# Optimization experiments

Hardware: AMD Instinct MI355X
Metric: run time of the kernel (lower is better)

Reference implementation:

```python
import jax, jax.numpy as jnp
import numpy as np

N = 100000
E = 600000
NODE_DIM = 128
EDGE_DIM = 32
HIDDEN = 128  # must equal NODE_DIM (index_add_ into zeros_like(node_features))


def _linear_params(key, fan_in, fan_out):
    kw, kb = jax.random.split(key)
    bound = 1.0 / np.sqrt(fan_in)
    W = jax.random.uniform(kw, (fan_in, fan_out), minval=-bound, maxval=bound, dtype=jnp.float32)
    b = jax.random.uniform(kb, (fan_out,), minval=-bound, maxval=bound, dtype=jnp.float32)
    return W, b


def setup_inputs() -> dict:
    key = jax.random.key(0)
    ks = jax.random.split(key, 8)
    node_features = jax.random.normal(ks[0], (N, NODE_DIM), dtype=jnp.float32)
    edge_index = jax.random.randint(ks[1], (2, E), 0, N, dtype=jnp.int32)
    edge_features = jax.random.normal(ks[2], (E, EDGE_DIM), dtype=jnp.float32)
    m_W1, m_b1 = _linear_params(ks[3], 2 * NODE_DIM + EDGE_DIM, HIDDEN)
    m_W2, m_b2 = _linear_params(ks[4], HIDDEN, HIDDEN)
    a_W, a_b = _linear_params(ks[5], HIDDEN, 1)
    u_W1, u_b1 = _linear_params(ks[6], NODE_DIM + HIDDEN, HIDDEN)
    u_W2, u_b2 = _linear_params(ks[7], HIDDEN, NODE_DIM)
    return {
        "node_features": node_features,
        "edge_features": edge_features,
        "m_W1": m_W1, "m_b1": m_b1, "m_W2": m_W2, "m_b2": m_b2,
        "a_W": a_W, "a_b": a_b,
        "u_W1": u_W1, "u_b1": u_b1, "u_W2": u_W2, "u_b2": u_b2,
        "edge_index": edge_index,
    }


def reference(node_features, edge_features, m_W1, m_b1, m_W2, m_b2,
              a_W, a_b, u_W1, u_b1, u_W2, u_b2, edge_index):
    row, col = edge_index[0], edge_index[1]
    # gather endpoints + edge feats -> [E, 2*node_dim + edge_dim]
    msg_in = jnp.concatenate([node_features[row], node_features[col], edge_features], axis=-1)
    # message MLP
    h = jax.nn.relu(msg_in @ m_W1 + m_b1)
    messages = h @ m_W2 + m_b2  # [E, hidden]
    # global softmax over all edges (dim=0), per attention column (width 1)
    attn = jax.nn.softmax(messages @ a_W + a_b, axis=0)  # [E, 1]
    messages = messages * attn
    # scatter-add into destination nodes
    aggregated = jax.ops.segment_sum(messages, col, num_segments=node_features.shape[0])
    # update MLP + residual
    upd_in = jnp.concatenate([node_features, aggregated], axis=-1)
    u = jax.nn.relu(upd_in @ u_W1 + u_b1)
    updated = u @ u_W2 + u_b2
    return updated + node_features
```

## Files before the change

kernel.cpp:

```cpp
#include <hip/hip_runtime.h>
#include <hip/hip_bf16.h>
#include <hip/hip_fp8.h>
#include <stdint.h>

#define NN 100000
#define NE 600000
#define ND 128
#define ED 32
#define HID 128
#define SCANB 391
#define NB (NE / 192)

using short8 = __attribute__((ext_vector_type(8))) short;
using f32x4  = __attribute__((ext_vector_type(4))) float;
using f32x2  = __attribute__((ext_vector_type(2))) float;

__device__ __forceinline__ uint32_t f2bf(float f) {
  uint32_t u = __float_as_uint(f);
  return (u + 0x7FFFu + ((u >> 16) & 1u)) >> 16;
}
__device__ __forceinline__ short8 pack8(float4 a, float4 b) {
  short8 s;
  s[0] = (short)f2bf(a.x); s[1] = (short)f2bf(a.y);
  s[2] = (short)f2bf(a.z); s[3] = (short)f2bf(a.w);
  s[4] = (short)f2bf(b.x); s[5] = (short)f2bf(b.y);
  s[6] = (short)f2bf(b.z); s[7] = (short)f2bf(b.w);
  return s;
}

__device__ __forceinline__ uint8_t fp8_enc(float v) {
#if __has_builtin(__builtin_amdgcn_cvt_pk_fp8_f32)
  return (uint8_t)(__builtin_amdgcn_cvt_pk_fp8_f32(v, v, 0, false) & 0xFF);
#else
  __hip_fp8_e4m3 q(v);
  return q.__x;
#endif
}
__device__ __forceinline__ float2 fp8_dec2(uint32_t v) {
#if __has_builtin(__builtin_amdgcn_cvt_pk_f32_fp8)
  f32x2 r = __builtin_amdgcn_cvt_pk_f32_fp8((int)v, false);
  return make_float2(r[0], r[1]);
#else
  __hip_fp8_e4m3 qa, qb;
  qa.__x = (uint8_t)(v & 0xFF); qb.__x = (uint8_t)((v >> 8) & 0xFF);
  return make_float2((float)qa, (float)qb);
#endif
}

__global__ __launch_bounds__(256) void k_prep(
    const float* __restrict__ W1, const float* __restrict__ W2,
    const float* __restrict__ uW1, const float* __restrict__ uW2,
    short* __restrict__ W1p, short* __restrict__ W2p,
    short* __restrict__ U1p, short* __restrict__ U2p) {
  int o = blockIdx.x * 256 + threadIdx.x;
  const float* src; short* dst; int rel;
  if (o < 36864)      { rel = o;         src = W1;  dst = W1p; }
  else if (o < 53248) { rel = o - 36864; src = W2;  dst = W2p; }
  else if (o < 86016) { rel = o - 53248; src = uW1; dst = U1p; }
  else                { rel = o - 86016; src = uW2; dst = U2p; }
  int j = rel & 7, c16 = (rel >> 3) & 15, g = (rel >> 7) & 3, nt = (rel >> 9) & 7, c = rel >> 12;
  int k = c * 32 + g * 8 + j, n = nt * 16 + c16;
  dst[rel] = (short)f2bf(src[k * 128 + n]);
}

__global__ __launch_bounds__(256) void k_prep_nf(const float* __restrict__ nf,
                                                 short* __restrict__ nfb) {
  const int total = NN * ND / 8;
  for (int u = blockIdx.x * 256 + threadIdx.x; u < total; u += gridDim.x * 256) {
    const float* s = nf + (size_t)u * 8;
    float4 v0 = *(const float4*)s, v1 = *(const float4*)(s + 4);
    *(short8*)(nfb + (size_t)u * 8) = pack8(v0, v1);
  }
}

__global__ __launch_bounds__(256, 2) void k_edge_mfma(
    const short* __restrict__ nfb, const float* __restrict__ ef,
    const short* __restrict__ W1p, const float* __restrict__ b1,
    const short* __restrict__ W2p, const float* __restrict__ b2,
    const float* __restrict__ aW, const int* __restrict__ ei,
    const int* __restrict__ perm,
    uint8_t* __restrict__ msg8, float* __restrict__ logits) {
  __shared__ __align__(16) short sA[192 * 40];
  __shared__ __align__(16) short sB[4096];
  __shared__ __align__(16) short sH[192 * 136];
  __shared__ int sIdx[384];
  __shared__ int sPerm[192];
  uint8_t* const sF = (uint8_t*)sH;

  const int tid = threadIdx.x;
  const int wv = tid >> 6, ln = tid & 63, cr = ln & 15, gp = ln >> 4;
  const int e0 = blockIdx.x * 192;
  const int wrow = wv * 48;

  if (tid < 192) {
    sIdx[tid] = ei[e0 + tid];
    sIdx[192 + tid] = ei[NE + e0 + tid];
    sPerm[tid] = perm[e0 + tid];
  }

  float bia[8], aWr[8], bia2[8];
#pragma unroll
  for (int nt = 0; nt < 8; ++nt) {
    bia[nt] = b1[nt * 16 + cr];
    bia2[nt] = b2[nt * 16 + cr];
    aWr[nt] = aW[nt * 16 + cr];
  }
  f32x4 acc[3][8];
#pragma unroll
  for (int mt = 0; mt < 3; ++mt)
#pragma unroll
    for (int nt = 0; nt < 8; ++nt)
      acc[mt][nt] = (f32x4){bia[nt], bia[nt], bia[nt], bia[nt]};
  __syncthreads();

  for (int c = 0; c < 9; ++c) {
#pragma unroll
    for (int it = 0; it < 3; ++it) {
      int row = it * 64 + (tid >> 2), k8 = (tid & 3) * 8;
      if (c < 8) {
        const short* src = nfb + (size_t)sIdx[(c < 4 ? 0 : 192) + row] * ND +
                           (c & 3) * 32 + k8;
        *(short8*)&sA[row * 40 + k8] = *(const short8*)src;
      } else {
        const float* src = ef + (size_t)(e0 + row) * ED + k8;
        float4 v0 = *(const float4*)src, v1 = *(const float4*)(src + 4);
        *(short8*)&sA[row * 40 + k8] = pack8(v0, v1);
      }
    }
    {
      const short8* wsrc = (const short8*)(W1p + c * 4096);
      short8 t0 = wsrc[tid], t1 = wsrc[tid + 256];
      ((short8*)sB)[tid] = t0; ((short8*)sB)[tid + 256] = t1;
    }
    __syncthreads();
    short8 af[3];
#pragma unroll
    for (int mt = 0; mt < 3; ++mt)
      af[mt] = *(const short8*)&sA[(wrow + mt * 16 + cr) * 40 + gp * 8];
#pragma unroll
    for (int nt = 0; nt < 8; ++nt) {
      short8 bfr = *(const short8*)&sB[(nt * 4 + gp) * 128 + cr * 8];
#pragma unroll
      for (int mt = 0; mt < 3; ++mt)
        acc[mt][nt] = __builtin_amdgcn_mfma_f32_16x16x32_bf16(af[mt], bfr, acc[mt][nt], 0, 0, 0);
    }
    __syncthreads();
  }

#pragma unroll
  for (int mt = 0; mt < 3; ++mt)
#pragma unroll
    for (int nt = 0; nt < 8; ++nt)
#pragma unroll
      for (int rr = 0; rr < 4; ++rr)
        sH[(wrow + mt * 16 + gp * 4 + rr) * 136 + nt * 16 + cr] =
            (short)f2bf(fmaxf(acc[mt][nt][rr], 0.f));
  __syncthreads();

  f32x4 acc2[3][8];
#pragma unroll
  for (int mt = 0; mt < 3; ++mt)
#pragma unroll
    for (int nt = 0; nt < 8; ++nt)
      acc2[mt][nt] = (f32x4){bia2[nt], bia2[nt], bia2[nt], bia2[nt]};
  for (int c2 = 0; c2 < 4; ++c2) {
    {
      const short8* wsrc = (const short8*)(W2p + c2 * 4096);
      short8 t0 = wsrc[tid], t1 = wsrc[tid + 256];
      ((short8*)sB)[tid] = t0; ((short8*)sB)[tid + 256] = t1;
    }
    __syncthreads();
    short8 af[3];
#pragma unroll
    for (int mt = 0; mt < 3; ++mt)
      af[mt] = *(const short8*)&sH[(wrow + mt * 16 + cr) * 136 + c2 * 32 + gp * 8];
#pragma unroll
    for (int nt = 0; nt < 8; ++nt) {
      short8 bfr = *(const short8*)&sB[(nt * 4 + gp) * 128 + cr * 8];
#pragma unroll
      for (int mt = 0; mt < 3; ++mt)
        acc2[mt][nt] = __builtin_amdgcn_mfma_f32_16x16x32_bf16(af[mt], bfr, acc2[mt][nt], 0, 0, 0);
    }
    __syncthreads();
  }

#pragma unroll
  for (int mt = 0; mt < 3; ++mt)
#pragma unroll
    for (int rr = 0; rr < 4; ++rr) {
      float p = 0.f;
#pragma unroll
      for (int nt = 0; nt < 8; ++nt) p += acc2[mt][nt][rr] * aWr[nt];
      p += __shfl_xor(p, 1, 64);
      p += __shfl_xor(p, 2, 64);
      p += __shfl_xor(p, 4, 64);
      p += __shfl_xor(p, 8, 64);
      if (cr == 0) logits[sPerm[wrow + mt * 16 + gp * 4 + rr]] = p;
    }

#pragma unroll
  for (int mt = 0; mt < 3; ++mt)
#pragma unroll
    for (int nt = 0; nt < 8; ++nt)
#pragma unroll
      for (int rr = 0; rr < 4; ++rr)
        sF[(wrow + mt * 16 + gp * 4 + rr) * 136 + nt * 16 + cr] =
            fp8_enc(acc2[mt][nt][rr]);
  __syncthreads();
#pragma unroll
  for (int it = 0; it < 12; ++it) {
    int row = it * 16 + (tid >> 4), o8 = (tid & 15) * 8;
    *(uint2*)(msg8 + (size_t)sPerm[row] * HID + o8) = *(const uint2*)&sF[row * 136 + o8];
  }
}

__global__ __launch_bounds__(256, 2) void k_node_mfma(
    const float* __restrict__ nf, const short* __restrict__ nfb,
    const float* __restrict__ agg,
    const short* __restrict__ U1p, const float* __restrict__ b1,
    const short* __restrict__ U2p, const float* __restrict__ b2,
    float* __restrict__ out) {
  __shared__ __align__(16) short sA[192 * 40];
  __shared__ __align__(16) short sB[4096];
  __shared__ __align__(16) short sH[192 * 136];

  const int tid = threadIdx.x;
  const int wv = tid >> 6, ln = tid & 63, cr = ln & 15, gp = ln >> 4;
  const int n0 = blockIdx.x * 192;
  const int wrow = wv * 48;

  float bia[8], bia2[8];
#pragma unroll
  for (int nt = 0; nt < 8; ++nt) {
    bia[nt] = b1[nt * 16 + cr];
    bia2[nt] = b2[nt * 16 + cr];
  }
  f32x4 acc[3][8];
#pragma unroll
  for (int mt = 0; mt < 3; ++mt)
#pragma unroll
    for (int nt = 0; nt < 8; ++nt)
      acc[mt][nt] = (f32x4){bia[nt], bia[nt], bia[nt], bia[nt]};

  for (int c = 0; c < 8; ++c) {
#pragma unroll
    for (int it = 0; it < 3; ++it) {
      int row = it * 64 + (tid >> 2), k8 = (tid & 3) * 8;
      int n = n0 + row; if (n >= NN) n = NN - 1;
      if (c < 4) {
        *(short8*)&sA[row * 40 + k8] =
            *(const short8*)(nfb + (size_t)n * ND + c * 32 + k8);
      } else {
        const float* src = agg + (size_t)n * ND + (c - 4) * 32 + k8;
        float4 v0 = *(const float4*)src, v1 = *(const float4*)(src + 4);
        *(short8*)&sA[row * 40 + k8] = pack8(v0, v1);
      }
    }
    {
      const short8* wsrc = (const short8*)(U1p + c * 4096);
      short8 t0 = wsrc[tid], t1 = wsrc[tid + 256];
      ((short8*)sB)[tid] = t0; ((short8*)sB)[tid + 256] = t1;
    }
    __syncthreads();
    short8 af[3];
#pragma unroll
    for (int mt = 0; mt < 3; ++mt)
      af[mt] = *(const short8*)&sA[(wrow + mt * 16 + cr) * 40 + gp * 8];
#pragma unroll
    for (int nt = 0; nt < 8; ++nt) {
      short8 bfr = *(const short8*)&sB[(nt * 4 + gp) * 128 + cr * 8];
#pragma unroll
      for (int mt = 0; mt < 3; ++mt)
        acc[mt][nt] = __builtin_amdgcn_mfma_f32_16x16x32_bf16(af[mt], bfr, acc[mt][nt], 0, 0, 0);
    }
    __syncthreads();
  }

#pragma unroll
  for (int mt = 0; mt < 3; ++mt)
#pragma unroll
    for (int nt = 0; nt < 8; ++nt)
#pragma unroll
      for (int rr = 0; rr < 4; ++rr)
        sH[(wrow + mt * 16 + gp * 4 + rr) * 136 + nt * 16 + cr] =
            (short)f2bf(fmaxf(acc[mt][nt][rr], 0.f));
  __syncthreads();

  f32x4 acc2[3][8];
#pragma unroll
  for (int mt = 0; mt < 3; ++mt)
#pragma unroll
    for (int nt = 0; nt < 8; ++nt)
      acc2[mt][nt] = (f32x4){bia2[nt], bia2[nt], bia2[nt], bia2[nt]};
  for (int c2 = 0; c2 < 4; ++c2) {
    {
      const short8* wsrc = (const short8*)(U2p + c2 * 4096);
      short8 t0 = wsrc[tid], t1 = wsrc[tid + 256];
      ((short8*)sB)[tid] = t0; ((short8*)sB)[tid + 256] = t1;
    }
    __syncthreads();
    short8 af[3];
#pragma unroll
    for (int mt = 0; mt < 3; ++mt)
      af[mt] = *(const short8*)&sH[(wrow + mt * 16 + cr) * 136 + c2 * 32 + gp * 8];
#pragma unroll
    for (int nt = 0; nt < 8; ++nt) {
      short8 bfr = *(const short8*)&sB[(nt * 4 + gp) * 128 + cr * 8];
#pragma unroll
      for (int mt = 0; mt < 3; ++mt)
        acc2[mt][nt] = __builtin_amdgcn_mfma_f32_16x16x32_bf16(af[mt], bfr, acc2[mt][nt], 0, 0, 0);
    }
    __syncthreads();
  }

#pragma unroll
  for (int mt = 0; mt < 3; ++mt)
#pragma unroll
    for (int rr = 0; rr < 4; ++rr) {
      int n = n0 + wrow + mt * 16 + gp * 4 + rr;
      if (n < NN) {
#pragma unroll
        for (int nt = 0; nt < 8; ++nt) {
          int col = nt * 16 + cr;
          out[(size_t)n * ND + col] = acc2[mt][nt][rr] + nf[(size_t)n * ND + col];
        }
      }
    }
}

__device__ __forceinline__ void ms_combine(float& m, float& s, float m2, float s2) {
  float M = fmaxf(m, m2);
  s = s * expf(m - M) + s2 * expf(m2 - M);
  m = M;
}
__device__ __forceinline__ void ms_block_reduce(float& m, float& s) {
#pragma unroll
  for (int o = 1; o < 64; o <<= 1) {
    float m2 = __shfl_xor(m, o, 64), s2 = __shfl_xor(s, o, 64);
    ms_combine(m, s, m2, s2);
  }
  __shared__ float sm[4], ss[4];
  if ((threadIdx.x & 63) == 0) { sm[threadIdx.x >> 6] = m; ss[threadIdx.x >> 6] = s; }
  __syncthreads();
  m = sm[0]; s = ss[0];
  ms_combine(m, s, sm[1], ss[1]);
  ms_combine(m, s, sm[2], ss[2]);
  ms_combine(m, s, sm[3], ss[3]);
}
__global__ __launch_bounds__(256) void k_red_p(const float* __restrict__ logits,
                                               float* __restrict__ pmax,
                                               float* __restrict__ psum) {
  float m = -3.402823466e38f, s = 0.f;
  for (int i = blockIdx.x * 256 + threadIdx.x; i < NE; i += 1024 * 256) {
    float l = logits[i];
    if (l <= m) s += expf(l - m);
    else { s = s * expf(m - l) + 1.f; m = l; }
  }
  ms_block_reduce(m, s);
  if (threadIdx.x == 0) { pmax[blockIdx.x] = m; psum[blockIdx.x] = s; }
}
__global__ __launch_bounds__(256) void k_red_f(const float* __restrict__ pmax,
                                               const float* __restrict__ psum,
                                               float* __restrict__ red) {
  float m = pmax[threadIdx.x], s = psum[threadIdx.x];
  ms_combine(m, s, pmax[threadIdx.x + 256], psum[threadIdx.x + 256]);
  ms_combine(m, s, pmax[threadIdx.x + 512], psum[threadIdx.x + 512]);
  ms_combine(m, s, pmax[threadIdx.x + 768], psum[threadIdx.x + 768]);
  ms_block_reduce(m, s);
  if (threadIdx.x == 0) { red[0] = m; red[1] = 1.0f / s; }
}

__global__ __launch_bounds__(256) void k_zero_cnt(int* __restrict__ cnt) {
  int i = blockIdx.x * 256 + threadIdx.x;
  if (i < NN) cnt[i] = 0;
}
__global__ __launch_bounds__(256) void k_hist(const int* __restrict__ ei,
                                              int* __restrict__ cnt) {
  int e = blockIdx.x * 256 + threadIdx.x;
  if (e < NE) atomicAdd(&cnt[ei[NE + e]], 1);
}
__global__ __launch_bounds__(256) void k_scan_bsum(const int* __restrict__ cnt,
                                                   int* __restrict__ bsum) {
  int i = blockIdx.x * 256 + threadIdx.x;
  int v = (i < NN) ? cnt[i] : 0;
#pragma unroll
  for (int s = 1; s < 64; s <<= 1) v += __shfl_xor(v, s, 64);
  __shared__ int sv[4];
  if ((threadIdx.x & 63) == 0) sv[threadIdx.x >> 6] = v;
  __syncthreads();
  if (threadIdx.x == 0) bsum[blockIdx.x] = sv[0] + sv[1] + sv[2] + sv[3];
}
__global__ __launch_bounds__(512) void k_scan_boff(const int* __restrict__ bsum,
                                                   int* __restrict__ boff,
                                                   int* __restrict__ rowptr) {
  __shared__ int s[512];
  int t = threadIdx.x;
  int v = (t < SCANB) ? bsum[t] : 0;
  s[t] = v;
  __syncthreads();
  for (int off = 1; off < 512; off <<= 1) {
    int u = (t >= off) ? s[t - off] : 0;
    __syncthreads();
    s[t] += u;
    __syncthreads();
  }
  if (t < SCANB) boff[t] = s[t] - v;
  if (t == 0) rowptr[NN] = NE;
}
__global__ __launch_bounds__(256) void k_scan_final(int* __restrict__ cnt,
                                                    const int* __restrict__ boff,
                                                    int* __restrict__ rowptr) {
  __shared__ int s[256];
  int b = blockIdx.x, t = threadIdx.x, i = b * 256 + t;
  int v = (i < NN) ? cnt[i] : 0;
  s[t] = v;
  __syncthreads();
  for (int off = 1; off < 256; off <<= 1) {
    int u = (t >= off) ? s[t - off] : 0;
    __syncthreads();
    s[t] += u;
    __syncthreads();
  }
  int excl = s[t] - v + boff[b];
  if (i < NN) { rowptr[i] = excl; cnt[i] = excl; }
}
__global__ __launch_bounds__(256) void k_fill(const int* __restrict__ ei,
                                              int* __restrict__ cursor,
                                              int* __restrict__ perm) {
  int e = blockIdx.x * 256 + threadIdx.x;
  if (e >= NE) return;
  int c = ei[NE + e];
  int pos = atomicAdd(&cursor[c], 1);
  perm[e] = pos;
}

__global__ __launch_bounds__(256) void k_agg(
    const uint8_t* __restrict__ msg8, const float* __restrict__ logits,
    const int* __restrict__ rowptr, const float* __restrict__ red,
    float* __restrict__ out) {
  int n = blockIdx.x * 4 + (threadIdx.x >> 6);
  int lane = threadIdx.x & 63;
  if (n >= NN) return;
  float gm = red[0], inv = red[1];
  int i0 = rowptr[n], i1 = rowptr[n + 1];
  float a0 = 0.f, a1 = 0.f;
  for (int i = i0; i < i1; ++i) {
    float wt = expf(logits[i] - gm) * inv;
    uint32_t pk = *(const uint16_t*)(msg8 + (size_t)i * HID + lane * 2);
    float2 d = fp8_dec2(pk);
    a0 += wt * d.x;
    a1 += wt * d.y;
  }
  *(float2*)(out + (size_t)n * ND + lane * 2) = make_float2(a0, a1);
}

extern "C" void kernel_launch(void* const* d_in, const int* in_sizes, int n_in,
                              void* d_out, int out_size, void* d_ws, size_t ws_size,
                              hipStream_t stream) {
  const float* nf  = (const float*)d_in[0];
  const float* ef  = (const float*)d_in[1];
  const float* mW1 = (const float*)d_in[2];
  const float* mb1 = (const float*)d_in[3];
  const float* mW2 = (const float*)d_in[4];
  const float* mb2 = (const float*)d_in[5];
  const float* aW  = (const float*)d_in[6];
  const float* uW1 = (const float*)d_in[8];
  const float* ub1 = (const float*)d_in[9];
  const float* uW2 = (const float*)d_in[10];
  const float* ub2 = (const float*)d_in[11];
  const int*   ei  = (const int*)d_in[12];
  float* out = (float*)d_out;

  char* ws = (char*)d_ws;
  uint8_t* msg8 = (uint8_t*)ws;
  float* logits = (float*)(ws + 76800000);
  float* pmax = (float*)(ws + 79200000);
  float* psum = pmax + 1024;
  float* red  = psum + 1024;
  short* W1p = (short*)(ws + 79208256);
  short* W2p = W1p + 36864;
  short* U1p = W2p + 16384;
  short* U2p = U1p + 32768;
  int* rowptr = (int*)(ws + 79413056);
  int* cnt    = rowptr + (NN + 1);
  int* perm   = cnt + NN;
  int* bsum   = perm + NE;
  int* boff   = bsum + 512;
  short* nfb  = (short*)(ws + 82620000);

  k_prep<<<400, 256, 0, stream>>>(mW1, mW2, uW1, uW2, W1p, W2p, U1p, U2p);
  k_prep_nf<<<2048, 256, 0, stream>>>(nf, nfb);
  k_zero_cnt<<<SCANB, 256, 0, stream>>>(cnt);
  k_hist<<<(NE + 255) / 256, 256, 0, stream>>>(ei, cnt);
  k_scan_bsum<<<SCANB, 256, 0, stream>>>(cnt, bsum);
  k_scan_boff<<<1, 512, 0, stream>>>(bsum, boff, rowptr);
  k_scan_final<<<SCANB, 256, 0, stream>>>(cnt, boff, rowptr);
  k_fill<<<(NE + 255) / 256, 256, 0, stream>>>(ei, cnt, perm);
  k_edge_mfma<<<NB, 256, 0, stream>>>(nfb, ef, W1p, mb1, W2p, mb2, aW, ei, perm,
                                      msg8, logits);
  k_red_p<<<1024, 256, 0, stream>>>(logits, pmax, psum);
  k_red_f<<<1, 256, 0, stream>>>(pmax, psum, red);
  k_agg<<<(NN + 3) / 4, 256, 0, stream>>>(msg8, logits, rowptr, red, out);
  k_node_mfma<<<(NN + 191) / 192, 256, 0, stream>>>(nf, nfb, out, U1p, ub1, U2p, ub2, out);
}
```

Before: 340.2 us.

## Switch edge message MLP to FP8 MFMA with prefetched gathers and double-buffered weights

The edge MLP now uses FP8 e4m3 inputs and weights with the 16x16x32 fp8 MFMA instead of bf16. An fp8 copy of the node features is written in the prep kernel, and the row and column gathers for all 192 edges are loaded into shared memory once up front. Weight chunks are double-buffered, which removes one barrier per K chunk. This halves gather bytes and LDS traffic, but adds an extra fp8 node-feature write and lowers the precision of the messages and hidden activations.

```diff
diff --git a/kernel.cpp b/kernel.cpp
--- a/kernel.cpp
+++ b/kernel.cpp
@@ -48,44 +48,59 @@
 }
 
 __global__ __launch_bounds__(256) void k_prep(
-    const float* __restrict__ W1, const float* __restrict__ W2,
     const float* __restrict__ uW1, const float* __restrict__ uW2,
-    short* __restrict__ W1p, short* __restrict__ W2p,
     short* __restrict__ U1p, short* __restrict__ U2p) {
   int o = blockIdx.x * 256 + threadIdx.x;
   const float* src; short* dst; int rel;
-  if (o < 36864)      { rel = o;         src = W1;  dst = W1p; }
-  else if (o < 53248) { rel = o - 36864; src = W2;  dst = W2p; }
-  else if (o < 86016) { rel = o - 53248; src = uW1; dst = U1p; }
-  else                { rel = o - 86016; src = uW2; dst = U2p; }
+  if (o < 32768)      { rel = o;         src = uW1; dst = U1p; }
+  else if (o < 49152) { rel = o - 32768; src = uW2; dst = U2p; }
+  else return;
   int j = rel & 7, c16 = (rel >> 3) & 15, g = (rel >> 7) & 3, nt = (rel >> 9) & 7, c = rel >> 12;
   int k = c * 32 + g * 8 + j, n = nt * 16 + c16;
   dst[rel] = (short)f2bf(src[k * 128 + n]);
 }
 
+__global__ __launch_bounds__(256) void k_prep8(
+    const float* __restrict__ W1, const float* __restrict__ W2,
+    uint8_t* __restrict__ W1p8, uint8_t* __restrict__ W2p8) {
+  int o = blockIdx.x * 256 + threadIdx.x;
+  const float* src; uint8_t* dst; int rel;
+  if (o < 36864)      { rel = o;         src = W1; dst = W1p8; }
+  else if (o < 53248) { rel = o - 36864; src = W2; dst = W2p8; }
+  else return;
+  int j = rel & 7, c16 = (rel >> 3) & 15, g = (rel >> 7) & 3, nt = (rel >> 9) & 7, c = rel >> 12;
+  int k = c * 32 + g * 8 + j, n = nt * 16 + c16;
+  dst[rel] = fp8_enc(src[k * 128 + n]);
+}
+
 __global__ __launch_bounds__(256) void k_prep_nf(const float* __restrict__ nf,
-                                                 short* __restrict__ nfb) {
+                                                 short* __restrict__ nfb,
+                                                 uint8_t* __restrict__ nfb8) {
   const int total = NN * ND / 8;
   for (int u = blockIdx.x * 256 + threadIdx.x; u < total; u += gridDim.x * 256) {
     const float* s = nf + (size_t)u * 8;
     float4 v0 = *(const float4*)s, v1 = *(const float4*)(s + 4);
     *(short8*)(nfb + (size_t)u * 8) = pack8(v0, v1);
+    uint8_t b[8];
+    b[0] = fp8_enc(v0.x); b[1] = fp8_enc(v0.y); b[2] = fp8_enc(v0.z); b[3] = fp8_enc(v0.w);
+    b[4] = fp8_enc(v1.x); b[5] = fp8_enc(v1.y); b[6] = fp8_enc(v1.z); b[7] = fp8_enc(v1.w);
+    *(uint2*)(nfb8 + (size_t)u * 8) = *(const uint2*)b;
   }
 }
 
 __global__ __launch_bounds__(256, 2) void k_edge_mfma(
-    const short* __restrict__ nfb, const float* __restrict__ ef,
-    const short* __restrict__ W1p, const float* __restrict__ b1,
-    const short* __restrict__ W2p, const float* __restrict__ b2,
+    const uint8_t* __restrict__ nfb8, const float* __restrict__ ef,
+    const uint8_t* __restrict__ W1p8, const float* __restrict__ b1,
+    const uint8_t* __restrict__ W2p8, const float* __restrict__ b2,
     const float* __restrict__ aW, const int* __restrict__ ei,
     const int* __restrict__ perm,
     uint8_t* __restrict__ msg8, float* __restrict__ logits) {
-  __shared__ __align__(16) short sA[192 * 40];
-  __shared__ __align__(16) short sB[4096];
-  __shared__ __align__(16) short sH[192 * 136];
+  __shared__ __align__(16) uint8_t sRow[192 * 136];
+  __shared__ __align__(16) uint8_t sCol[192 * 136];
+  __shared__ __align__(16) uint8_t sEf[192 * 40];
+  __shared__ __align__(16) uint8_t sB8[2][4096];
   __shared__ int sIdx[384];
   __shared__ int sPerm[192];
-  uint8_t* const sF = (uint8_t*)sH;
 
   const int tid = threadIdx.x;
   const int wv = tid >> 6, ln = tid & 63, cr = ln & 15, gp = ln >> 4;
@@ -97,6 +112,30 @@
     sIdx[192 + tid] = ei[NE + e0 + tid];
     sPerm[tid] = perm[e0 + tid];
   }
+  __syncthreads();
+
+#pragma unroll
+  for (int it = 0; it < 24; ++it) {
+    int t = it * 256 + tid;
+    int side = t >= 3072;
+    int r = (t - side * 3072) >> 4;
+    int o = (t & 15) * 8;
+    const uint8_t* src = nfb8 + (size_t)sIdx[side * 192 + r] * ND + o;
+    uint8_t* dst = (side ? sCol : sRow) + r * 136 + o;
+    *(uint2*)dst = *(const uint2*)src;
+  }
+#pragma unroll
+  for (int it = 0; it < 3; ++it) {
+    int u = it * 256 + tid;
+    int r = u >> 2, o = (u & 3) * 8;
+    const float* src = ef + (size_t)(e0 + r) * ED + o;
+    float4 v0 = *(const float4*)src, v1 = *(const float4*)(src + 4);
+    uint8_t b[8];
+    b[0] = fp8_enc(v0.x); b[1] = fp8_enc(v0.y); b[2] = fp8_enc(v0.z); b[3] = fp8_enc(v0.w);
+    b[4] = fp8_enc(v1.x); b[5] = fp8_enc(v1.y); b[6] = fp8_enc(v1.z); b[7] = fp8_enc(v1.w);
+    *(uint2*)&sEf[r * 40 + o] = *(const uint2*)b;
+  }
+  *(uint4*)&sB8[0][tid * 16] = *(const uint4*)(W1p8 + tid * 16);
 
   float bia[8], aWr[8], bia2[8];
 #pragma unroll
@@ -114,35 +153,22 @@
   __syncthreads();
 
   for (int c = 0; c < 9; ++c) {
-#pragma unroll
-    for (int it = 0; it < 3; ++it) {
-      int row = it * 64 + (tid >> 2), k8 = (tid & 3) * 8;
-      if (c < 8) {
-        const short* src = nfb + (size_t)sIdx[(c < 4 ? 0 : 192) + row] * ND +
-                           (c & 3) * 32 + k8;
-        *(short8*)&sA[row * 40 + k8] = *(const short8*)src;
-      } else {
-        const float* src = ef + (size_t)(e0 + row) * ED + k8;
-        float4 v0 = *(const float4*)src, v1 = *(const float4*)(src + 4);
-        *(short8*)&sA[row * 40 + k8] = pack8(v0, v1);
-      }
-    }
-    {
-      const short8* wsrc = (const short8*)(W1p + c * 4096);
-      short8 t0 = wsrc[tid], t1 = wsrc[tid + 256];
-      ((short8*)sB)[tid] = t0; ((short8*)sB)[tid + 256] = t1;
-    }
-    __syncthreads();
-    short8 af[3];
-#pragma unroll
-    for (int mt = 0; mt < 3; ++mt)
-      af[mt] = *(const short8*)&sA[(wrow + mt * 16 + cr) * 40 + gp * 8];
+    if (c < 8)
+      *(uint4*)&sB8[(c + 1) & 1][tid * 16] =
+          *(const uint4*)(W1p8 + (c + 1) * 4096 + tid * 16);
+    const uint8_t* aSrc = (c < 4) ? (sRow + c * 32)
+                        : (c < 8) ? (sCol + (c - 4) * 32) : sEf;
+    const int pitch = (c == 8) ? 40 : 136;
+    long af0 = *(const long*)(aSrc + (wrow + cr) * pitch + gp * 8);
+    long af1 = *(const long*)(aSrc + (wrow + 16 + cr) * pitch + gp * 8);
+    long af2 = *(const long*)(aSrc + (wrow + 32 + cr) * pitch + gp * 8);
+    const uint8_t* bbuf = sB8[c & 1];
 #pragma unroll
     for (int nt = 0; nt < 8; ++nt) {
-      short8 bfr = *(const short8*)&sB[(nt * 4 + gp) * 128 + cr * 8];
-#pragma unroll
-      for (int mt = 0; mt < 3; ++mt)
-        acc[mt][nt] = __builtin_amdgcn_mfma_f32_16x16x32_bf16(af[mt], bfr, acc[mt][nt], 0, 0, 0);
+      long bfr = *(const long*)&bbuf[(nt * 4 + gp) * 128 + cr * 8];
+      acc[0][nt] = __builtin_amdgcn_mfma_f32_16x16x32_fp8_fp8(af0, bfr, acc[0][nt], 0, 0, 0);
+      acc[1][nt] = __builtin_amdgcn_mfma_f32_16x16x32_fp8_fp8(af1, bfr, acc[1][nt], 0, 0, 0);
+      acc[2][nt] = __builtin_amdgcn_mfma_f32_16x16x32_fp8_fp8(af2, bfr, acc[2][nt], 0, 0, 0);
     }
     __syncthreads();
   }
@@ -153,8 +179,9 @@
     for (int nt = 0; nt < 8; ++nt)
 #pragma unroll
       for (int rr = 0; rr < 4; ++rr)
-        sH[(wrow + mt * 16 + gp * 4 + rr) * 136 + nt * 16 + cr] =
-            (short)f2bf(fmaxf(acc[mt][nt][rr], 0.f));
+        sRow[(wrow + mt * 16 + gp * 4 + rr) * 136 + nt * 16 + cr] =
+            fp8_enc(fmaxf(acc[mt][nt][rr], 0.f));
+  *(uint4*)&sB8[0][tid * 16] = *(const uint4*)(W2p8 + tid * 16);
   __syncthreads();
 
   f32x4 acc2[3][8];
@@ -164,22 +191,19 @@
     for (int nt = 0; nt < 8; ++nt)
       acc2[mt][nt] = (f32x4){bia2[nt], bia2[nt], bia2[nt], bia2[nt]};
   for (int c2 = 0; c2 < 4; ++c2) {
-    {
-      const short8* wsrc = (const short8*)(W2p + c2 * 4096);
-      short8 t0 = wsrc[tid], t1 = wsrc[tid + 256];
-      ((short8*)sB)[tid] = t0; ((short8*)sB)[tid + 256] = t1;
-    }
-    __syncthreads();
-    short8 af[3];
-#pragma unroll
-    for (int mt = 0; mt < 3; ++mt)
-      af[mt] = *(const short8*)&sH[(wrow + mt * 16 + cr) * 136 + c2 * 32 + gp * 8];
+    if (c2 < 3)
+      *(uint4*)&sB8[(c2 + 1) & 1][tid * 16] =
+          *(const uint4*)(W2p8 + (c2 + 1) * 4096 + tid * 16);
+    long af0 = *(const long*)&sRow[(wrow + cr) * 136 + c2 * 32 + gp * 8];
+    long af1 = *(const long*)&sRow[(wrow + 16 + cr) * 136 + c2 * 32 + gp * 8];
+    long af2 = *(const long*)&sRow[(wrow + 32 + cr) * 136 + c2 * 32 + gp * 8];
+    const uint8_t* bbuf = sB8[c2 & 1];
 #pragma unroll
     for (int nt = 0; nt < 8; ++nt) {
-      short8 bfr = *(const short8*)&sB[(nt * 4 + gp) * 128 + cr * 8];
-#pragma unroll
-      for (int mt = 0; mt < 3; ++mt)
-        acc2[mt][nt] = __builtin_amdgcn_mfma_f32_16x16x32_bf16(af[mt], bfr, acc2[mt][nt], 0, 0, 0);
+      long bfr = *(const long*)&bbuf[(nt * 4 + gp) * 128 + cr * 8];
+      acc2[0][nt] = __builtin_amdgcn_mfma_f32_16x16x32_fp8_fp8(af0, bfr, acc2[0][nt], 0, 0, 0);
+      acc2[1][nt] = __builtin_amdgcn_mfma_f32_16x16x32_fp8_fp8(af1, bfr, acc2[1][nt], 0, 0, 0);
+      acc2[2][nt] = __builtin_amdgcn_mfma_f32_16x16x32_fp8_fp8(af2, bfr, acc2[2][nt], 0, 0, 0);
     }
     __syncthreads();
   }
@@ -204,13 +228,13 @@
     for (int nt = 0; nt < 8; ++nt)
 #pragma unroll
       for (int rr = 0; rr < 4; ++rr)
-        sF[(wrow + mt * 16 + gp * 4 + rr) * 136 + nt * 16 + cr] =
+        sCol[(wrow + mt * 16 + gp * 4 + rr) * 136 + nt * 16 + cr] =
             fp8_enc(acc2[mt][nt][rr]);
   __syncthreads();
 #pragma unroll
   for (int it = 0; it < 12; ++it) {
     int row = it * 16 + (tid >> 4), o8 = (tid & 15) * 8;
-    *(uint2*)(msg8 + (size_t)sPerm[row] * HID + o8) = *(const uint2*)&sF[row * 136 + o8];
+    *(uint2*)(msg8 + (size_t)sPerm[row] * HID + o8) = *(const uint2*)&sCol[row * 136 + o8];
   }
 }
 
@@ -477,9 +501,9 @@
   float* pmax = (float*)(ws + 79200000);
   float* psum = pmax + 1024;
   float* red  = psum + 1024;
-  short* W1p = (short*)(ws + 79208256);
-  short* W2p = W1p + 36864;
-  short* U1p = W2p + 16384;
+  uint8_t* W1p8 = (uint8_t*)(ws + 79208256);
+  uint8_t* W2p8 = W1p8 + 36864;
+  short* U1p = (short*)(W2p8 + 16384);
   short* U2p = U1p + 32768;
   int* rowptr = (int*)(ws + 79413056);
   int* cnt    = rowptr + (NN + 1);
@@ -487,16 +511,18 @@
   int* bsum   = perm + NE;
   int* boff   = bsum + 512;
   short* nfb  = (short*)(ws + 82620000);
-
-  k_prep<<<400, 256, 0, stream>>>(mW1, mW2, uW1, uW2, W1p, W2p, U1p, U2p);
-  k_prep_nf<<<2048, 256, 0, stream>>>(nf, nfb);
+  uint8_t* nfb8 = (uint8_t*)(ws + 108220000);
+
+  k_prep<<<192, 256, 0, stream>>>(uW1, uW2, U1p, U2p);
+  k_prep8<<<208, 256, 0, stream>>>(mW1, mW2, W1p8, W2p8);
+  k_prep_nf<<<2048, 256, 0, stream>>>(nf, nfb, nfb8);
   k_zero_cnt<<<SCANB, 256, 0, stream>>>(cnt);
   k_hist<<<(NE + 255) / 256, 256, 0, stream>>>(ei, cnt);
   k_scan_bsum<<<SCANB, 256, 0, stream>>>(cnt, bsum);
   k_scan_boff<<<1, 512, 0, stream>>>(bsum, boff, rowptr);
   k_scan_final<<<SCANB, 256, 0, stream>>>(cnt, boff, rowptr);
   k_fill<<<(NE + 255) / 256, 256, 0, stream>>>(ei, cnt, perm);
-  k_edge_mfma<<<NB, 256, 0, stream>>>(nfb, ef, W1p, mb1, W2p, mb2, aW, ei, perm,
+  k_edge_mfma<<<NB, 256, 0, stream>>>(nfb8, ef, W1p8, mb1, W2p8, mb2, aW, ei, perm,
                                       msg8, logits);
   k_red_p<<<1024, 256, 0, stream>>>(logits, pmax, psum);
   k_red_f<<<1, 256, 0, stream>>>(pmax, psum, red);
```

New measurement: 334.9 us. No clear change (-1.6%).
